# Kernel optimization log

Hardware: AMD Instinct MI355X
Metric: run time of the kernel (lower is better)

The kernel has to match this reference:

```python
import jax, jax.numpy as jnp
import numpy as np

N = 50000      # nodes
E = 800000     # edges (avg degree 16)
F_IN = 128     # num_node_features
D = 64         # embedding_size (= per-head out_channels)
H = 4          # heads
ED = 20        # edge_dim (hardcoded in module)
SLOPE = 0.2    # GATv2 leaky_relu negative slope
N_LAYERS = 3   # conv applied 3 times with shared weights


def setup_inputs() -> dict:
    key = jax.random.key(0)
    ks = jax.random.split(key, 12)
    s = 0.1
    return {
        "x": jax.random.normal(ks[0], (N, F_IN), jnp.float32),
        "edge_attr": jax.random.normal(ks[1], (E, 2), jnp.float32),
        "edge_index": jax.random.randint(ks[2], (2, E), 0, N, dtype=jnp.int32),
        # f: Linear(F_IN, D)
        "f_W": jax.random.normal(ks[3], (F_IN, D), jnp.float32) * s,
        "f_b": jnp.zeros((D,), jnp.float32),
        # fe: Linear(2, ED)
        "fe_W": jax.random.normal(ks[4], (2, ED), jnp.float32) * s,
        "fe_b": jnp.zeros((ED,), jnp.float32),
        # GATv2Conv lin_l / lin_r: Linear(D, H*D)
        "Wl": jax.random.normal(ks[5], (D, H * D), jnp.float32) * s,
        "bl": jnp.zeros((H * D,), jnp.float32),
        "Wr": jax.random.normal(ks[6], (D, H * D), jnp.float32) * s,
        "br": jnp.zeros((H * D,), jnp.float32),
        # lin_edge: Linear(ED, H*D, bias=False)
        "We": jax.random.normal(ks[7], (ED, H * D), jnp.float32) * s,
        # attention vector att: [H, D]
        "att": jax.random.normal(ks[8], (H, D), jnp.float32) * s,
        # final bias (concat=False -> size D)
        "bias": jnp.zeros((D,), jnp.float32),
    }


def _gatv2_conv(h, e_emb, src, dst, Wl, bl, Wr, br, We, att, bias):
    # h: [N, D], e_emb: [E, ED], src/dst: [E]
    xl = (h @ Wl + bl).reshape(-1, H, D)        # source transform  [N,H,D]
    xr = (h @ Wr + br).reshape(-1, H, D)        # target transform  [N,H,D]
    ee = (e_emb @ We).reshape(-1, H, D)         # edge transform    [E,H,D]
    m = jax.nn.leaky_relu(xl[src] + xr[dst] + ee, SLOPE)  # [E,H,D]
    score = jnp.einsum('ehd,hd->eh', m, att)    # [E,H]
    # segment softmax over incoming edges of each dst node
    smax = jax.ops.segment_max(score, dst, num_segments=N)   # [N,H]
    ex = jnp.exp(score - smax[dst])
    denom = jax.ops.segment_sum(ex, dst, num_segments=N)     # [N,H]
    alpha = ex / denom[dst]                                  # [E,H]
    out = jax.ops.segment_sum(alpha[:, :, None] * xl[src], dst, num_segments=N)  # [N,H,D]
    return out.mean(axis=1) + bias              # concat=False -> head mean, [N,D]


def reference(x, edge_attr, edge_index, f_W, f_b, fe_W, fe_b, Wl, bl, Wr, br, We, att, bias):
    src, dst = edge_index[0], edge_index[1]
    h = jax.nn.relu(x @ f_W + f_b)
    e = jax.nn.relu(edge_attr @ fe_W + fe_b)
    for _ in range(N_LAYERS):
        h = jax.nn.relu(_gatv2_conv(h, e, src, dst, Wl, bl, Wr, br, We, att, bias))
    return h
```

## Files before the change

### kernel.cpp

```cpp
#include <hip/hip_runtime.h>
#include <math.h>

typedef float v2f __attribute__((ext_vector_type(2)));

#define LN2_INV 1.4426950408889634f

__device__ __forceinline__ float fexp2(float x) {
#if __has_builtin(__builtin_amdgcn_exp2f)
    return __builtin_amdgcn_exp2f(x);
#else
    return exp2f(x);
#endif
}

__device__ __forceinline__ int rdlane_i(int v, int k) {
    return __builtin_amdgcn_readlane(v, k);
}

#define DPP_ROW_ADD(V, CTRL) \
    V += __int_as_float(__builtin_amdgcn_update_dpp(0, __float_as_int(V), CTRL, 0xf, 0xf, true));

__global__ __launch_bounds__(256) void k_h0(const float* __restrict__ x,
                                            const float* __restrict__ fW,
                                            const float* __restrict__ fb,
                                            float* __restrict__ h0) {
    __shared__ __align__(16) float xs[8 * 128];
    int t = threadIdx.x;
    int base = blockIdx.x * 8;
#pragma unroll
    for (int r = 0; r < 4; ++r) { int j = r * 256 + t; xs[j] = x[base * 128 + j]; }
    __syncthreads();
    int c = t & 63, half = t >> 6;
    float acc0 = fb[c], acc1 = fb[c];
    int m0 = half, m1 = half + 4;
#pragma unroll 8
    for (int k0 = 0; k0 < 128; k0 += 4) {
        float4 a = *(const float4*)&xs[m0 * 128 + k0];
        float4 b = *(const float4*)&xs[m1 * 128 + k0];
        float w0 = fW[(k0 + 0) * 64 + c], w1 = fW[(k0 + 1) * 64 + c];
        float w2 = fW[(k0 + 2) * 64 + c], w3 = fW[(k0 + 3) * 64 + c];
        acc0 = fmaf(a.x, w0, fmaf(a.y, w1, fmaf(a.z, w2, fmaf(a.w, w3, acc0))));
        acc1 = fmaf(b.x, w0, fmaf(b.y, w1, fmaf(b.z, w2, fmaf(b.w, w3, acc1))));
    }
    h0[(base + m0) * 64 + c] = fmaxf(acc0, 0.f);
    h0[(base + m1) * 64 + c] = fmaxf(acc1, 0.f);
}

__global__ __launch_bounds__(256) void k_xlxr(const float* __restrict__ h,
                                              const float* __restrict__ Wl,
                                              const float* __restrict__ Wr,
                                              const float* __restrict__ bl,
                                              const float* __restrict__ br,
                                              float* __restrict__ xl,
                                              float* __restrict__ xr) {
    __shared__ __align__(16) float hs[16 * 64];
    int t = threadIdx.x;
    int base = blockIdx.x * 16;
#pragma unroll
    for (int r = 0; r < 4; ++r) hs[r * 256 + t] = h[base * 64 + r * 256 + t];
    __syncthreads();
    float bL = bl[t], bR = br[t];
    float accl[16], accr[16];
#pragma unroll
    for (int m = 0; m < 16; ++m) { accl[m] = bL; accr[m] = bR; }
#pragma unroll 4
    for (int k0 = 0; k0 < 64; k0 += 4) {
        float wl[4], wr[4];
#pragma unroll
        for (int q = 0; q < 4; ++q) {
            wl[q] = Wl[(k0 + q) * 256 + t];
            wr[q] = Wr[(k0 + q) * 256 + t];
        }
#pragma unroll
        for (int m = 0; m < 16; ++m) {
            float4 hv = *(const float4*)&hs[m * 64 + k0];
            accl[m] = fmaf(hv.x, wl[0], fmaf(hv.y, wl[1], fmaf(hv.z, wl[2], fmaf(hv.w, wl[3], accl[m]))));
            accr[m] = fmaf(hv.x, wr[0], fmaf(hv.y, wr[1], fmaf(hv.z, wr[2], fmaf(hv.w, wr[3], accr[m]))));
        }
    }
#pragma unroll
    for (int m = 0; m < 16; ++m) {
        xl[(base + m) * 256 + t] = accl[m];
        xr[(base + m) * 256 + t] = accr[m];
    }
}

__global__ void k_zero(int* __restrict__ deg, int* __restrict__ counter, int Nn) {
    int i = blockIdx.x * 256 + threadIdx.x;
    if (i < Nn) deg[i] = 0;
    if (i == 0) *counter = 0;
}

__global__ void k_count(const int* __restrict__ dstArr, int* __restrict__ deg, int Ee) {
    int e = blockIdx.x * 256 + threadIdx.x;
    if (e < Ee) atomicAdd(&deg[dstArr[e]], 1);
}

__global__ void k_alloc(const int* __restrict__ deg, int* __restrict__ counter,
                        int* __restrict__ start, int* __restrict__ cursor, int Nn) {
    int n = blockIdx.x * 256 + threadIdx.x;
    if (n < Nn) {
        int d = deg[n];
        int b = atomicAdd(counter, d);
        start[n] = b;
        cursor[n] = b;
    }
}

__global__ void k_fill(const int* __restrict__ dstArr, const int* __restrict__ srcArr,
                       const float* __restrict__ eattr, const float* __restrict__ feW,
                       const float* __restrict__ feb, int* __restrict__ cursor,
                       int* __restrict__ rec, int Ee) {
    int e = blockIdx.x * 256 + threadIdx.x;
    if (e >= Ee) return;
    float a0 = eattr[2 * e], a1 = eattr[2 * e + 1];
    int p = atomicAdd(&cursor[dstArr[e]], 1);
    float* r = (float*)(rec + (size_t)p * 24);
    float s[20];
#pragma unroll
    for (int k = 0; k < 20; ++k)
        s[k] = fmaxf(fmaf(a0, feW[k], fmaf(a1, feW[20 + k], feb[k])), 0.f);
#pragma unroll
    for (int j = 0; j < 5; ++j)
        ((float4*)r)[j] = make_float4(s[4 * j], s[4 * j + 1], s[4 * j + 2], s[4 * j + 3]);
    ((int*)r)[20] = srcArr[e];
}

__global__ __launch_bounds__(256, 3) void k_edge(
    const float4* __restrict__ xl4p, const float4* __restrict__ xr4p,
    const float* __restrict__ att, const float4* __restrict__ We4,
    const int* __restrict__ rec, const int* __restrict__ start,
    const int* __restrict__ deg, const float* __restrict__ bias,
    float* __restrict__ hout, int Nn) {
    __shared__ __align__(16) float4 swe[20 * 64];
    const int t = threadIdx.x;
#pragma unroll
    for (int j = 0; j < 5; ++j) swe[j * 256 + t] = We4[j * 256 + t];
    __syncthreads();

    const int lane = t & 63;
    const int n = (int)((blockIdx.x * 256u + t) >> 6);
    if (n >= Nn) return;

    const int dn = __builtin_amdgcn_readfirstlane(deg[n]);
    float4 bias4 = ((const float4*)bias)[lane & 15];
    if (dn == 0) {
        if (lane < 16) {
            float4 o = make_float4(fmaxf(bias4.x, 0.f), fmaxf(bias4.y, 0.f),
                                   fmaxf(bias4.z, 0.f), fmaxf(bias4.w, 0.f));
            ((float4*)hout)[(size_t)n * 16 + lane] = o;
        }
        return;
    }
    const int s0 = __builtin_amdgcn_readfirstlane(start[n]);
    const int* rb = rec + (size_t)s0 * 24 + (lane & 31);

    float4 attv = ((const float4*)att)[lane];
    float4 aA = make_float4(0.6f * LN2_INV * attv.x, 0.6f * LN2_INV * attv.y,
                            0.6f * LN2_INV * attv.z, 0.6f * LN2_INV * attv.w);
    float4 aB = make_float4(0.4f * LN2_INV * attv.x, 0.4f * LN2_INV * attv.y,
                            0.4f * LN2_INV * attv.z, 0.4f * LN2_INV * attv.w);
    float4 xrv = xr4p[(size_t)n * 64 + lane];
    v2f xr01 = {xrv.x, xrv.y}, xr23 = {xrv.z, xrv.w};
    const int bperm = ((lane & 48) | 15) << 2;

    v2f acc01 = {0.f, 0.f}, acc23 = {0.f, 0.f};
    float l = 0.f;

    const int nfull = dn >> 2;
    const int rem = dn & 3;
    const int ngroups = nfull + (rem ? 1 : 0);
    const int fb = dn >= 4 ? dn - 4 : 0;

#define LOAD_GROUP(RV, B)                                                   \
    {                                                                       \
        _Pragma("unroll")                                                   \
        for (int j_ = 0; j_ < 4; ++j_) {                                    \
            int idx_ = (B) + j_;                                            \
            idx_ = idx_ < dn ? idx_ : dn - 1;                               \
            RV[j_] = rb[(size_t)idx_ * 24];                                 \
        }                                                                   \
    }
#define GATHER_GROUP(XL, RV)                                                \
    {                                                                       \
        _Pragma("unroll")                                                   \
        for (int j_ = 0; j_ < 4; ++j_) {                                    \
            int src_ = rdlane_i(RV[j_], 20);                                \
            XL[j_] = xl4p[(size_t)src_ * 64 + lane];                        \
        }                                                                   \
    }

    int rvA[4], rvB[4];
    float4 xlA[4], xlB[4];
    int b0 = (nfull > 0) ? 0 : fb;
    LOAD_GROUP(rvA, b0)
    GATHER_GROUP(xlA, rvA)

    for (int g = 0; g < ngroups; ++g) {
        int gn = g + 1;
        bool havenext = gn < ngroups;
        if (havenext) {
            int bn = (gn < nfull) ? (gn << 2) : fb;
            LOAD_GROUP(rvB, bn)
        }

        v2f ee01[4], ee23[4];
        {
            float4 w = swe[lane];
            v2f w01 = {w.x, w.y}, w23 = {w.z, w.w};
#pragma unroll
            for (int j = 0; j < 4; ++j) {
                float sk = __int_as_float(rdlane_i(rvA[j], 0));
                ee01[j] = sk * w01;
                ee23[j] = sk * w23;
            }
        }
#pragma unroll
        for (int k = 1; k < 20; ++k) {
            float4 w = swe[k * 64 + lane];
            v2f w01 = {w.x, w.y}, w23 = {w.z, w.w};
#pragma unroll
            for (int j = 0; j < 4; ++j) {
                float sk = __int_as_float(rdlane_i(rvA[j], k));
                ee01[j] += sk * w01;
                ee23[j] += sk * w23;
            }
        }

        if (havenext) GATHER_GROUP(xlB, rvB)

        int b = (g < nfull) ? (g << 2) : fb;
        int lo = (g < nfull) ? b : (nfull << 2);
        float ps[4];
#pragma unroll
        for (int j = 0; j < 4; ++j) {
            v2f v01 = {xlA[j].x, xlA[j].y};
            v2f v23 = {xlA[j].z, xlA[j].w};
            v01 = (v01 + xr01) + ee01[j];
            v23 = (v23 + xr23) + ee23[j];
            float tt = aB.x * __builtin_fabsf(v01.x);
            tt = fmaf(aA.x, v01.x, tt);
            tt = fmaf(aB.y, __builtin_fabsf(v01.y), tt);
            tt = fmaf(aA.y, v01.y, tt);
            tt = fmaf(aB.z, __builtin_fabsf(v23.x), tt);
            tt = fmaf(aA.z, v23.x, tt);
            tt = fmaf(aB.w, __builtin_fabsf(v23.y), tt);
            tt = fmaf(aA.w, v23.y, tt);
            ps[j] = tt;
        }
#pragma unroll
        for (int j = 0; j < 4; ++j) { DPP_ROW_ADD(ps[j], 0x111) }
#pragma unroll
        for (int j = 0; j < 4; ++j) { DPP_ROW_ADD(ps[j], 0x112) }
#pragma unroll
        for (int j = 0; j < 4; ++j) { DPP_ROW_ADD(ps[j], 0x114) }
#pragma unroll
        for (int j = 0; j < 4; ++j) { DPP_ROW_ADD(ps[j], 0x118) }
#pragma unroll
        for (int j = 0; j < 4; ++j) {
            float sc = __int_as_float(
                __builtin_amdgcn_ds_bpermute(bperm, __float_as_int(ps[j])));
            float mk = (b + j >= lo && b + j < dn) ? 1.f : 0.f;
            float w_ = fexp2(sc) * mk;
            l += w_;
            v2f xl01 = {xlA[j].x, xlA[j].y};
            v2f xl23 = {xlA[j].z, xlA[j].w};
            acc01 += w_ * xl01;
            acc23 += w_ * xl23;
        }

        if (havenext) {
#pragma unroll
            for (int j = 0; j < 4; ++j) { rvA[j] = rvB[j]; xlA[j] = xlB[j]; }
        }
    }
#undef LOAD_GROUP
#undef GATHER_GROUP

    float inv = 0.25f / l;
    float4 r = make_float4(acc01.x * inv, acc01.y * inv, acc23.x * inv, acc23.y * inv);
    r.x += __shfl_xor(r.x, 16, 64); r.x += __shfl_xor(r.x, 32, 64);
    r.y += __shfl_xor(r.y, 16, 64); r.y += __shfl_xor(r.y, 32, 64);
    r.z += __shfl_xor(r.z, 16, 64); r.z += __shfl_xor(r.z, 32, 64);
    r.w += __shfl_xor(r.w, 16, 64); r.w += __shfl_xor(r.w, 32, 64);
    if (lane < 16) {
        float4 o = make_float4(fmaxf(r.x + bias4.x, 0.f), fmaxf(r.y + bias4.y, 0.f),
                               fmaxf(r.z + bias4.z, 0.f), fmaxf(r.w + bias4.w, 0.f));
        ((float4*)hout)[(size_t)n * 16 + lane] = o;
    }
}

extern "C" void kernel_launch(void* const* d_in, const int* in_sizes, int n_in,
                              void* d_out, int out_size, void* d_ws, size_t ws_size,
                              hipStream_t stream) {
    const float* x     = (const float*)d_in[0];
    const float* eattr = (const float*)d_in[1];
    const int*   eidx  = (const int*)d_in[2];
    const float* fW    = (const float*)d_in[3];
    const float* fb    = (const float*)d_in[4];
    const float* feW   = (const float*)d_in[5];
    const float* feb   = (const float*)d_in[6];
    const float* Wl    = (const float*)d_in[7];
    const float* bl    = (const float*)d_in[8];
    const float* Wr    = (const float*)d_in[9];
    const float* br    = (const float*)d_in[10];
    const float* We    = (const float*)d_in[11];
    const float* att   = (const float*)d_in[12];
    const float* bias  = (const float*)d_in[13];
    float* out = (float*)d_out;

    const int N = in_sizes[0] / 128;
    const int E = in_sizes[1] / 2;
    const int* srcArr = eidx;
    const int* dstArr = eidx + E;

    char* p = (char*)d_ws;
    auto alloc = [&](size_t bytes) -> char* {
        char* r = p;
        p += (bytes + 255) & ~(size_t)255;
        return r;
    };
    float* hA   = (float*)alloc((size_t)N * 64 * 4);
    float* hB   = (float*)alloc((size_t)N * 64 * 4);
    float* xl   = (float*)alloc((size_t)N * 256 * 4);
    float* xr   = (float*)alloc((size_t)N * 256 * 4);
    int* deg    = (int*)alloc((size_t)N * 4);
    int* start  = (int*)alloc((size_t)N * 4);
    int* cursor = (int*)alloc((size_t)N * 4);
    int* counter = (int*)alloc(256);
    int* rec    = (int*)alloc((size_t)E * 24 * 4 + 256);

    k_h0<<<N / 8, 256, 0, stream>>>(x, fW, fb, hA);
    k_zero<<<(N + 255) / 256, 256, 0, stream>>>(deg, counter, N);
    k_count<<<(E + 255) / 256, 256, 0, stream>>>(dstArr, deg, E);
    k_alloc<<<(N + 255) / 256, 256, 0, stream>>>(deg, counter, start, cursor, N);
    k_fill<<<(E + 255) / 256, 256, 0, stream>>>(dstArr, srcArr, eattr, feW, feb,
                                                cursor, rec, E);

    const float* hin = hA;
    for (int layer = 0; layer < 3; ++layer) {
        float* hout = (layer == 2) ? out : ((layer == 0) ? hB : hA);
        k_xlxr<<<N / 16, 256, 0, stream>>>(hin, Wl, Wr, bl, br, xl, xr);
        k_edge<<<(N * 64) / 256, 256, 0, stream>>>(
            (const float4*)xl, (const float4*)xr, att, (const float4*)We,
            rec, start, deg, bias, hout, N);
        hin = hout;
    }
}
```

Before: 1.089 ms.

## Drop LDS weight staging and simplify edge-group software pipeline

Removes the per-block LDS copy of the edge weight matrix and reads We directly from global/cache, dropping the __syncthreads. The two-stage prefetch of xl gathers is replaced with a simpler scheme that only prefetches the next group's records and gathers the current group's xl at loop start. Tail handling changes from an overlapping last group with a mask to per-edge branches. This cuts register pressure and LDS use but exposes gather latency and adds scalar branches in the inner loop.

```diff
diff --git a/kernel.cpp b/kernel.cpp
--- a/kernel.cpp
+++ b/kernel.cpp
@@ -132,14 +132,8 @@
     const int* __restrict__ rec, const int* __restrict__ start,
     const int* __restrict__ deg, const float* __restrict__ bias,
     float* __restrict__ hout, int Nn) {
-    __shared__ __align__(16) float4 swe[20 * 64];
-    const int t = threadIdx.x;
-#pragma unroll
-    for (int j = 0; j < 5; ++j) swe[j * 256 + t] = We4[j * 256 + t];
-    __syncthreads();
-
-    const int lane = t & 63;
-    const int n = (int)((blockIdx.x * 256u + t) >> 6);
+    const int lane = threadIdx.x & 63;
+    const int n = (int)((blockIdx.x * 256u + threadIdx.x) >> 6);
     if (n >= Nn) return;
 
     const int dn = __builtin_amdgcn_readfirstlane(deg[n]);
@@ -167,46 +161,35 @@
     v2f acc01 = {0.f, 0.f}, acc23 = {0.f, 0.f};
     float l = 0.f;
 
-    const int nfull = dn >> 2;
-    const int rem = dn & 3;
-    const int ngroups = nfull + (rem ? 1 : 0);
-    const int fb = dn >= 4 ? dn - 4 : 0;
-
-#define LOAD_GROUP(RV, B)                                                   \
-    {                                                                       \
-        _Pragma("unroll")                                                   \
-        for (int j_ = 0; j_ < 4; ++j_) {                                    \
-            int idx_ = (B) + j_;                                            \
-            idx_ = idx_ < dn ? idx_ : dn - 1;                               \
-            RV[j_] = rb[(size_t)idx_ * 24];                                 \
-        }                                                                   \
-    }
-#define GATHER_GROUP(XL, RV)                                                \
-    {                                                                       \
-        _Pragma("unroll")                                                   \
-        for (int j_ = 0; j_ < 4; ++j_) {                                    \
-            int src_ = rdlane_i(RV[j_], 20);                                \
-            XL[j_] = xl4p[(size_t)src_ * 64 + lane];                        \
-        }                                                                   \
-    }
+    const int ngroups = (dn + 3) >> 2;
 
     int rvA[4], rvB[4];
-    float4 xlA[4], xlB[4];
-    int b0 = (nfull > 0) ? 0 : fb;
-    LOAD_GROUP(rvA, b0)
-    GATHER_GROUP(xlA, rvA)
+#pragma unroll
+    for (int j = 0; j < 4; ++j) {
+        int idx = j < dn ? j : dn - 1;
+        rvA[j] = rb[(size_t)idx * 24];
+    }
 
     for (int g = 0; g < ngroups; ++g) {
-        int gn = g + 1;
-        bool havenext = gn < ngroups;
-        if (havenext) {
-            int bn = (gn < nfull) ? (gn << 2) : fb;
-            LOAD_GROUP(rvB, bn)
+        const int b = g << 2;
+
+        float4 xl[4];
+#pragma unroll
+        for (int j = 0; j < 4; ++j) {
+            int src = rdlane_i(rvA[j], 20);
+            xl[j] = xl4p[(size_t)src * 64 + lane];
+        }
+
+#pragma unroll
+        for (int j = 0; j < 4; ++j) {
+            int idx = b + 4 + j;
+            idx = idx < dn ? idx : dn - 1;
+            rvB[j] = rb[(size_t)idx * 24];
         }
 
         v2f ee01[4], ee23[4];
         {
-            float4 w = swe[lane];
+            float4 w = We4[lane];
             v2f w01 = {w.x, w.y}, w23 = {w.z, w.w};
 #pragma unroll
             for (int j = 0; j < 4; ++j) {
@@ -217,7 +200,7 @@
         }
 #pragma unroll
         for (int k = 1; k < 20; ++k) {
-            float4 w = swe[k * 64 + lane];
+            float4 w = We4[k * 64 + lane];
             v2f w01 = {w.x, w.y}, w23 = {w.z, w.w};
 #pragma unroll
             for (int j = 0; j < 4; ++j) {
@@ -227,55 +210,37 @@
             }
         }
 
-        if (havenext) GATHER_GROUP(xlB, rvB)
-
-        int b = (g < nfull) ? (g << 2) : fb;
-        int lo = (g < nfull) ? b : (nfull << 2);
-        float ps[4];
 #pragma unroll
         for (int j = 0; j < 4; ++j) {
-            v2f v01 = {xlA[j].x, xlA[j].y};
-            v2f v23 = {xlA[j].z, xlA[j].w};
-            v01 = (v01 + xr01) + ee01[j];
-            v23 = (v23 + xr23) + ee23[j];
-            float tt = aB.x * __builtin_fabsf(v01.x);
-            tt = fmaf(aA.x, v01.x, tt);
-            tt = fmaf(aB.y, __builtin_fabsf(v01.y), tt);
-            tt = fmaf(aA.y, v01.y, tt);
-            tt = fmaf(aB.z, __builtin_fabsf(v23.x), tt);
-            tt = fmaf(aA.z, v23.x, tt);
-            tt = fmaf(aB.w, __builtin_fabsf(v23.y), tt);
-            tt = fmaf(aA.w, v23.y, tt);
-            ps[j] = tt;
-        }
-#pragma unroll
-        for (int j = 0; j < 4; ++j) { DPP_ROW_ADD(ps[j], 0x111) }
-#pragma unroll
-        for (int j = 0; j < 4; ++j) { DPP_ROW_ADD(ps[j], 0x112) }
-#pragma unroll
-        for (int j = 0; j < 4; ++j) { DPP_ROW_ADD(ps[j], 0x114) }
-#pragma unroll
-        for (int j = 0; j < 4; ++j) { DPP_ROW_ADD(ps[j], 0x118) }
-#pragma unroll
-        for (int j = 0; j < 4; ++j) {
-            float sc = __int_as_float(
-                __builtin_amdgcn_ds_bpermute(bperm, __float_as_int(ps[j])));
-            float mk = (b + j >= lo && b + j < dn) ? 1.f : 0.f;
-            float w_ = fexp2(sc) * mk;
-            l += w_;
-            v2f xl01 = {xlA[j].x, xlA[j].y};
-            v2f xl23 = {xlA[j].z, xlA[j].w};
-            acc01 += w_ * xl01;
-            acc23 += w_ * xl23;
-        }
-
-        if (havenext) {
-#pragma unroll
-            for (int j = 0; j < 4; ++j) { rvA[j] = rvB[j]; xlA[j] = xlB[j]; }
-        }
-    }
-#undef LOAD_GROUP
-#undef GATHER_GROUP
+            if (b + j < dn) {
+                v2f xl01 = {xl[j].x, xl[j].y};
+                v2f xl23 = {xl[j].z, xl[j].w};
+                v2f v01 = (xl01 + xr01) + ee01[j];
+                v2f v23 = (xl23 + xr23) + ee23[j];
+                float tt = aB.x * __builtin_fabsf(v01.x);
+                tt = fmaf(aA.x, v01.x, tt);
+                tt = fmaf(aB.y, __builtin_fabsf(v01.y), tt);
+                tt = fmaf(aA.y, v01.y, tt);
+                tt = fmaf(aB.z, __builtin_fabsf(v23.x), tt);
+                tt = fmaf(aA.z, v23.x, tt);
+                tt = fmaf(aB.w, __builtin_fabsf(v23.y), tt);
+                tt = fmaf(aA.w, v23.y, tt);
+                DPP_ROW_ADD(tt, 0x111)
+                DPP_ROW_ADD(tt, 0x112)
+                DPP_ROW_ADD(tt, 0x114)
+                DPP_ROW_ADD(tt, 0x118)
+                float sc = __int_as_float(
+                    __builtin_amdgcn_ds_bpermute(bperm, __float_as_int(tt)));
+                float w_ = fexp2(sc);
+                l += w_;
+                acc01 += w_ * xl01;
+                acc23 += w_ * xl23;
+            }
+        }
+
+#pragma unroll
+        for (int j = 0; j < 4; ++j) rvA[j] = rvB[j];
+    }
 
     float inv = 0.25f / l;
     float4 r = make_float4(acc01.x * inv, acc01.y * inv, acc23.x * inv, acc23.y * inv);
```

Result: faster. 1.052 ms (-3.4%).
